# Kernel optimization log

Hardware: AMD Instinct MI355X
Metric: run time of the kernel (lower is better)

The kernel has to match this reference:

```python
import jax, jax.numpy as jnp
import numpy as np

H, N_EMB, D_EMB, D_UP = 1024, 8192, 512, 2048
B, T, BB, M, K_LABELS = 4, 4096, 512, 4096, 64


def _rms(x, w, eps=1e-6):
    xf = x.astype(jnp.float32)
    var = jnp.mean(xf * xf, axis=-1, keepdims=True)
    return (w * (xf * jax.lax.rsqrt(var + eps))).astype(x.dtype)


def setup_inputs() -> dict:
    key = jax.random.key(0)
    ks = jax.random.split(key, 8)
    bt = B * T
    inp = jax.random.normal(ks[0], (B, T, H), jnp.float32)
    w_k = jax.random.normal(ks[1], (N_EMB, H), jnp.float32) * 0.02
    w_v = jax.random.normal(ks[2], (N_EMB, D_EMB), jnp.float32) * 0.02
    w_up = jax.random.normal(ks[3], (D_UP, D_EMB), jnp.float32) * 0.02
    w_mix = jax.random.normal(ks[4], (H, D_UP + H), jnp.float32) * 0.02
    fw = jax.random.permutation(ks[5], bt)
    bw = jnp.argsort(fw)  # inverse permutation
    seq_sort = jax.random.randint(ks[6], (bt,), 0, K_LABELS)
    keep_cols = jnp.arange(M)  # keep first M of N_EMB rows
    emb_alloc = jnp.arange(N_EMB) % K_LABELS  # every label present among kept rows
    starts = jnp.zeros((bt,), jnp.int32)
    ends = jnp.full((bt,), M, jnp.int32)
    return {
        'input': inp, 'fw': fw, 'bw': bw, 'seq_sort': seq_sort,
        'keep_cols': keep_cols, 'emb_alloc': emb_alloc,
        'starts': starts, 'ends': ends, 'bb': BB,
        'w_k_weight': w_k, 'w_v_weight': w_v, 'w_up_weight': w_up,
        'w_mix_weight': w_mix,
        'norm_in_weight': jnp.ones((H,), jnp.float32),
        'norm_out_weight': jnp.ones((D_UP,), jnp.float32),
    }


def reference(input, fw, bw, seq_sort, keep_cols, emb_alloc, starts, ends, bb,
              w_k_weight, w_v_weight, w_up_weight, w_mix_weight,
              norm_in_weight, norm_out_weight):
    b, t, h = input.shape
    A = _rms(input, norm_in_weight)                      # [b,t,h]
    Bm = w_k_weight[keep_cols]                           # [m,h]
    Cm = w_v_weight[keep_cols]                           # [m,d_emb]
    la = emb_alloc[keep_cols]                            # [m]
    A = A.reshape(-1, h)[fw].reshape(-1, bb, h)          # [nb,bb,h]
    ss = seq_sort.reshape(-1, bb)                        # [nb,bb]
    st = starts.reshape(-1, bb).min(axis=-1)             # [nb]
    en = ends.reshape(-1, bb).max(axis=-1)               # [nb]
    # ragged per-block slice B[start:end] expressed as a kv range mask,
    # combined with the equality mask seq_sort[q] == emb_alloc[kv]
    scores = jnp.einsum('nqh,kh->nqk', A, Bm)            # [nb,bb,m]
    kv = jnp.arange(Bm.shape[0])
    mask = ((ss[:, :, None] == la[None, None, :])
            & (kv[None, None, :] >= st[:, None, None])
            & (kv[None, None, :] < en[:, None, None]))
    scores = jnp.where(mask, scores, -jnp.inf)
    p = jax.nn.softmax(scores, axis=-1)
    comb = jnp.einsum('nqk,kd->nqd', p, Cm)              # [nb,bb,d_emb]
    d_emb = Cm.shape[-1]
    comb = comb.reshape(-1, d_emb)[bw].reshape(b, t, d_emb)
    up = comb @ w_up_weight.T                            # [b,t,d_up]
    cat = jnp.concatenate([_rms(up, norm_out_weight), input], axis=-1)
    return cat @ w_mix_weight.T                          # [b,t,h]
```

## Files before the change

kernel.cpp:

```cpp
#include <hip/hip_runtime.h>
#include <hip/hip_bf16.h>
#include <cstdint>
#include <cstddef>

#define Hh 1024
#define D_EMB 512
#define D_UP 2048
#define BT 16384
#define BB_ 512
#define Mm 4096
#define NB 32
#define KL 64
#define NXCD 8
#define PMMAX 8192
#define QROWMAX 17408
#define MAXT 1088

typedef __attribute__((ext_vector_type(4))) float f4;
typedef __attribute__((ext_vector_type(4))) __bf16 bf4;
typedef __attribute__((ext_vector_type(8))) __bf16 bf8;
typedef __attribute__((ext_vector_type(4))) float f32x4;

__device__ __forceinline__ void gl_lds16(const void* g, void* l) {
  __builtin_amdgcn_global_load_lds((__attribute__((address_space(1))) void*)g,
                                   (__attribute__((address_space(3))) void*)l, 16, 0, 0);
}

__global__ __launch_bounds__(256) void conv_bf16_kernel(const float* __restrict__ src,
                                                        __bf16* __restrict__ dst, int n4) {
  int i = blockIdx.x * 256 + threadIdx.x;
  if (i >= n4) return;
  f4 v = ((const f4*)src)[i];
  bf4 o = {(__bf16)v[0], (__bf16)v[1], (__bf16)v[2], (__bf16)v[3]};
  ((bf4*)dst)[i] = o;
}

__global__ __launch_bounds__(256) void la_kernel(const int* __restrict__ keep,
                                                 const int* __restrict__ emb,
                                                 int* __restrict__ la, int m) {
  int i = blockIdx.x * 256 + threadIdx.x;
  if (i < m) la[i] = emb[keep[i]];
}

__global__ __launch_bounds__(256) void range_kernel(const int* __restrict__ starts,
                                                    const int* __restrict__ ends,
                                                    int* __restrict__ stA, int* __restrict__ enA) {
  int n = blockIdx.x;
  int t = threadIdx.x, lane = t & 63, wv = t >> 6;
  int s1 = min(starts[n * BB_ + t], starts[n * BB_ + t + 256]);
  int e1 = max(ends[n * BB_ + t], ends[n * BB_ + t + 256]);
#pragma unroll
  for (int off = 32; off; off >>= 1) {
    s1 = min(s1, __shfl_xor(s1, off));
    e1 = max(e1, __shfl_xor(e1, off));
  }
  __shared__ int ssh[4], esh[4];
  if (lane == 0) { ssh[wv] = s1; esh[wv] = e1; }
  __syncthreads();
  if (t == 0) {
    int s = ssh[0], e = esh[0];
#pragma unroll
    for (int k = 1; k < 4; ++k) { s = min(s, ssh[k]); e = max(e, esh[k]); }
    stA[n] = s; enA[n] = e;
  }
}

__global__ __launch_bounds__(256) void hist_kernel(const int* __restrict__ la,
                                                   int* __restrict__ goff) {
  __shared__ int cnt[KL];
  int tid = threadIdx.x;
  if (tid < KL) cnt[tid] = 0;
  __syncthreads();
  for (int k = tid; k < Mm; k += 256) atomicAdd(&cnt[la[k]], 1);
  __syncthreads();
  if (tid == 0) {
    int a = 0;
    for (int s = 0; s < KL; ++s) { goff[s] = a; a += cnt[s]; }
    goff[KL] = a;
  }
}

__global__ __launch_bounds__(256) void place_kernel(const int* __restrict__ la,
                                                    const int* __restrict__ keep,
                                                    const int* __restrict__ goff,
                                                    int* __restrict__ gk,
                                                    int* __restrict__ ridx) {
  int s = blockIdx.x;
  int tid = threadIdx.x, lane = tid & 63, wv = tid >> 6;
  __shared__ int wc[4];
  __shared__ int run;
  if (tid == 0) run = goff[s];
  __syncthreads();
  for (int base = 0; base < Mm; base += 256) {
    int k = base + tid;
    bool f = (la[k] == s);
    unsigned long long msk = __ballot(f);
    int myidx = __popcll(msk & ((1ull << lane) - 1ull));
    if (lane == 0) wc[wv] = __popcll(msk);
    __syncthreads();
    int woff = 0, tot = 0;
#pragma unroll
    for (int w = 0; w < 4; ++w) {
      if (w < wv) woff += wc[w];
      tot += wc[w];
    }
    int rbase = run;
    if (f) {
      int p = rbase + woff + myidx;
      gk[p] = k;
      ridx[p] = keep[k];
    }
    __syncthreads();
    if (tid == 0) run = rbase + tot;
    __syncthreads();
  }
}

__global__ __launch_bounds__(256) void qsort_kernel(const int* __restrict__ seq_sort,
                                                    int* __restrict__ qidx,
                                                    int* __restrict__ qoffA,
                                                    int* __restrict__ qcntA) {
  int n = blockIdx.x, tid = threadIdx.x;
  __shared__ int cnt[KL], pos[KL], pref[KL];
  if (tid < KL) cnt[tid] = 0;
  __syncthreads();
  int s0 = seq_sort[n * BB_ + tid];
  int s1 = seq_sort[n * BB_ + tid + 256];
  atomicAdd(&cnt[s0], 1);
  atomicAdd(&cnt[s1], 1);
  __syncthreads();
  if (tid == 0) {
    int a = 0;
    for (int s = 0; s < KL; ++s) { pref[s] = a; a += cnt[s]; }
  }
  __syncthreads();
  if (tid < KL) {
    pos[tid] = pref[tid];
    qoffA[n * KL + tid] = pref[tid];
    qcntA[n * KL + tid] = cnt[tid];
  }
  __syncthreads();
  int p0 = atomicAdd(&pos[s0], 1);
  qidx[n * BB_ + p0] = n * BB_ + tid;
  int p1 = atomicAdd(&pos[s1], 1);
  qidx[n * BB_ + p1] = n * BB_ + tid + 256;
}

__global__ __launch_bounds__(256) void qmeta_kernel(const int* __restrict__ qcntA,
                                                    const int* __restrict__ goff,
                                                    int* __restrict__ boff,
                                                    int* __restrict__ qtot,
                                                    int* __restrict__ ptq,
                                                    int* __restrict__ pb,
                                                    int* __restrict__ taskS,
                                                    int* __restrict__ taskT,
                                                    int* __restrict__ ntt,
                                                    int* __restrict__ pbTot) {
  int tid = threadIdx.x;
  if (tid < KL) {
    int s = tid, tot = 0;
    for (int n = 0; n < NB; ++n) { boff[n * KL + s] = tot; tot += qcntA[n * KL + s]; }
    qtot[s] = tot;
  }
  __syncthreads();
  if (tid == 0) {
    int tb = 0, tk = 0, pk = 0;
    for (int s = 0; s < KL; ++s) {
      ptq[s] = tb;
      int nt = (qtot[s] + 15) >> 4;
      for (int t2 = 0; t2 < nt; ++t2) { taskS[tk] = s; taskT[tk] = t2; ++tk; }
      tb += nt;
      pb[s] = pk;
      int cnt = goff[s + 1] - goff[s];
      pk += (cnt + 63) & ~63;
    }
    ptq[KL] = tb;
    ntt[0] = tk;
    pbTot[0] = pk;
  }
}

__global__ __launch_bounds__(256) void pridx_kernel(const int* __restrict__ goff,
                                                    const int* __restrict__ pb,
                                                    const int* __restrict__ ridx,
                                                    int* __restrict__ pridx) {
  int s = blockIdx.x;
  int cnt = goff[s + 1] - goff[s];
  int padded = (cnt + 63) & ~63;
  int base = pb[s];
  for (int i = threadIdx.x; i < padded; i += 256)
    pridx[base + i] = (i < cnt) ? ridx[goff[s] + i] : -1;
}

__global__ __launch_bounds__(256) void lohi_kernel(const int* __restrict__ gk,
                                                   const int* __restrict__ goff,
                                                   const int* __restrict__ pb,
                                                   const int* __restrict__ stA,
                                                   const int* __restrict__ enA,
                                                   int* __restrict__ loA, int* __restrict__ hiA) {
  int i = blockIdx.x * 256 + threadIdx.x;
  if (i >= NB * KL) return;
  int n = i / KL, s = i % KL;
  int b = goff[s], e = goff[s + 1];
  int st = stA[n], en = enA[n];
  int lo = b, hi = e;
  while (lo < hi) { int mid = (lo + hi) >> 1; if (gk[mid] < st) lo = mid + 1; else hi = mid; }
  int L = lo;
  lo = b; hi = e;
  while (lo < hi) { int mid = (lo + hi) >> 1; if (gk[mid] < en) lo = mid + 1; else hi = mid; }
  loA[i] = pb[s] + (L - goff[s]);
  hiA[i] = pb[s] + (lo - goff[s]);
}

__global__ __launch_bounds__(256) void gq_kernel(const int* __restrict__ qidx,
                                                 const int* __restrict__ qoffA,
                                                 const int* __restrict__ seq_sort,
                                                 const int* __restrict__ boff,
                                                 const int* __restrict__ ptq,
                                                 int* __restrict__ qg2, int* __restrict__ gq) {
  int e = blockIdx.x * 256 + threadIdx.x;
  int n = e >> 9;
  int q = qidx[e];
  int s = seq_sort[q];
  int i = (e & 511) - qoffA[n * KL + s];
  int gpos = ptq[s] * 16 + boff[n * KL + s] + i;
  qg2[gpos] = q;
  gq[q] = gpos;
}

__global__ __launch_bounds__(256) void qzero_kernel(const int* __restrict__ ptq,
                                                    const int* __restrict__ qtot,
                                                    __bf16* __restrict__ Qsw) {
  int s = blockIdx.x;
  int b0 = ptq[s] * 16 + qtot[s];
  int b1 = ptq[s + 1] * 16;
  bf8 z;
#pragma unroll
  for (int j = 0; j < 8; ++j) z[j] = (__bf16)0.f;
  for (int r = b0; r < b1; ++r)
    for (int e8 = threadIdx.x; e8 < 128; e8 += 256)
      *(bf8*)&Qsw[(size_t)r * 1024 + e8 * 8] = z;
}

__global__ __launch_bounds__(256) void kswb_kernel(const float* __restrict__ wk,
                                                   const int* __restrict__ pridx,
                                                   const int* __restrict__ pbTot,
                                                   __bf16* __restrict__ Ksw) {
  int pt = blockIdx.x;
  if (pt * 16 >= pbTot[0]) return;
  __shared__ __bf16 Tk[16][1040];
  int tid = threadIdx.x;
  int rr = tid >> 4, lt = tid & 15;
  int src = pridx[pt * 16 + rr];
  for (int cc = 0; cc < 16; ++cc) {
    int i4 = cc * 16 + lt;
    f4 v = {0.f, 0.f, 0.f, 0.f};
    if (src >= 0) v = ((const f4*)(wk + (size_t)src * Hh))[i4];
    bf4 o = {(__bf16)v[0], (__bf16)v[1], (__bf16)v[2], (__bf16)v[3]};
    *(bf4*)&Tk[rr][i4 * 4] = o;
  }
  __syncthreads();
#pragma unroll
  for (int i = 0; i < 8; ++i) {
    int f = tid + 256 * i;
    int ks = f >> 6, ln = f & 63;
    int c2 = ln & 15, rg2 = ln >> 4;
    bf8 o = *(const bf8*)&Tk[c2][ks * 32 + rg2 * 8];
    *(bf8*)&Ksw[(size_t)pt * 16384 + (size_t)f * 8] = o;
  }
}

__global__ __launch_bounds__(256) void vswb_kernel(const float* __restrict__ wv_,
                                                   const int* __restrict__ pridx,
                                                   const int* __restrict__ pbTot,
                                                   __bf16* __restrict__ Vsw) {
  int pblk = blockIdx.x;
  if (pblk * 32 >= pbTot[0]) return;
  __shared__ __bf16 Tv[32][528];
  int tid = threadIdx.x;
  int rr = tid >> 3, lt = tid & 7;
  int src = pridx[pblk * 32 + rr];
  for (int cc = 0; cc < 16; ++cc) {
    int i4 = cc * 8 + lt;
    f4 v = {0.f, 0.f, 0.f, 0.f};
    if (src >= 0) v = ((const f4*)(wv_ + (size_t)src * D_EMB))[i4];
    bf4 o = {(__bf16)v[0], (__bf16)v[1], (__bf16)v[2], (__bf16)v[3]};
    *(bf4*)&Tv[rr][i4 * 4] = o;
  }
  __syncthreads();
#pragma unroll
  for (int i = 0; i < 8; ++i) {
    int f = tid + 256 * i;
    int ff = f >> 6, ln = f & 63;
    int c2 = ln & 15, rg2 = ln >> 4;
    bf8 o;
#pragma unroll
    for (int j = 0; j < 8; ++j) o[j] = Tv[rg2 * 8 + j][ff * 16 + c2];
    *(bf8*)&Vsw[(size_t)pblk * 16384 + (size_t)f * 8] = o;
  }
}

__global__ __launch_bounds__(256) void rms_in_kernel(const float* __restrict__ input,
                                                     const int* __restrict__ bw,
                                                     const int* __restrict__ gq,
                                                     const float* __restrict__ wn,
                                                     __bf16* __restrict__ Qsw,
                                                     __bf16* __restrict__ inb) {
  __shared__ __align__(16) __bf16 rowbuf[4][1024];
  int wv = threadIdx.x >> 6, lane = threadIdx.x & 63;
  int j = blockIdx.x * 4 + wv;
  const f4* src = (const f4*)(input + (size_t)j * Hh);
  f4 v[4];
  float ss = 0.f;
#pragma unroll
  for (int c = 0; c < 4; ++c) {
    v[c] = src[c * 64 + lane];
    ss += v[c][0] * v[c][0] + v[c][1] * v[c][1] + v[c][2] * v[c][2] + v[c][3] * v[c][3];
  }
#pragma unroll
  for (int off = 32; off; off >>= 1) ss += __shfl_xor(ss, off);
  float sc = rsqrtf(ss * (1.f / Hh) + 1e-6f);
  bf4* dstI = (bf4*)(inb + (size_t)j * Hh);
#pragma unroll
  for (int c = 0; c < 4; ++c) {
    bf4 o = {(__bf16)v[c][0], (__bf16)v[c][1], (__bf16)v[c][2], (__bf16)v[c][3]};
    dstI[c * 64 + lane] = o;
  }
  const f4* w4 = (const f4*)wn;
#pragma unroll
  for (int c = 0; c < 4; ++c) {
    f4 w = w4[c * 64 + lane];
    bf4 o = {(__bf16)(v[c][0] * sc * w[0]), (__bf16)(v[c][1] * sc * w[1]),
             (__bf16)(v[c][2] * sc * w[2]), (__bf16)(v[c][3] * sc * w[3])};
    *(bf4*)&rowbuf[wv][(c * 64 + lane) * 4] = o;
  }
  int gpos = gq[bw[j]];
  int qt2 = gpos >> 4, cq = gpos & 15;
#pragma unroll
  for (int h = 0; h < 2; ++h) {
    int k_ = lane + h * 64;
    int ks = k_ >> 2, rg2 = k_ & 3;
    bf8 o = *(const bf8*)&rowbuf[wv][ks * 32 + rg2 * 8];
    *(bf8*)(Qsw + (size_t)qt2 * 16384 + ks * 512 + (cq + 16 * rg2) * 8) = o;
  }
}

__global__ __launch_bounds__(256, 3) void attn7_kernel(const __bf16* __restrict__ Qsw,
                                                       const __bf16* __restrict__ Ksw,
                                                       const __bf16* __restrict__ Vsw,
                                                       const int* __restrict__ qg2,
                                                       const int* __restrict__ qtot,
                                                       const int* __restrict__ ptq,
                                                       const int* __restrict__ taskS,
                                                       const int* __restrict__ taskT,
                                                       const int* __restrict__ nttA,
                                                       const int* __restrict__ pb,
                                                       const int* __restrict__ loP,
                                                       const int* __restrict__ hiP,
                                                       const int* __restrict__ fw,
                                                       __bf16* __restrict__ comb) {
  __shared__ float Sb[16][66];
  __shared__ __align__(16) __bf16 Plds[16][72];
  __shared__ float scl_s[16], lrec[16];
  __shared__ __align__(16) __bf16 owb[16][528];
  int t = blockIdx.x;
  if (t >= nttA[0]) return;
  int tid = threadIdx.x, wv = tid >> 6, lane = tid & 63;
  int c = lane & 15, rg = lane >> 4;
  int s = taskS[t], tl = taskT[t];
  int qtp = ptq[s] + tl;
  int qcnt = min(16, qtot[s] - tl * 16);
  bool qv = c < qcnt;
  int q_l = qg2[qtp * 16 + (qv ? c : 0)];
  int n_l = q_l >> 9;
  int lo_l = qv ? loP[n_l * KL + s] : 0x7fffffff;
  int hi_l = qv ? hiP[n_l * KL + s] : 0;
  int tlo = lo_l, thi = hi_l;
#pragma unroll
  for (int off = 1; off < 64; off <<= 1) {
    tlo = min(tlo, __shfl_xor(tlo, off));
    thi = max(thi, __shfl_xor(thi, off));
  }
  if (tlo >= thi) return;
  int pbs = pb[s];
  const __bf16* Qb = Qsw + (size_t)qtp * 16384 + lane * 8;

  float m[4] = {-1e30f, -1e30f, -1e30f, -1e30f};
  float l[4] = {0.f, 0.f, 0.f, 0.f};
  f32x4 acc[8];
  f32x4 zero = {0.f, 0.f, 0.f, 0.f};
#pragma unroll
  for (int tt = 0; tt < 8; ++tt) acc[tt] = zero;

  int p0beg = pbs + ((tlo - pbs) & ~63);
  for (int p0 = p0beg; p0 < thi; p0 += 64) {
    const __bf16* Kb = Ksw + (size_t)((p0 >> 4) + wv) * 16384 + lane * 8;
    f32x4 sacc = zero;
#pragma unroll
    for (int ks = 0; ks < 32; ++ks) {
      bf8 qf = *(const bf8*)(Qb + ks * 512);
      bf8 kf = *(const bf8*)(Kb + ks * 512);
      sacc = __builtin_amdgcn_mfma_f32_16x16x32_bf16(kf, qf, sacc, 0, 0, 0);
    }
#pragma unroll
    for (int r = 0; r < 4; ++r) {
      int kv = p0 + wv * 16 + rg * 4 + r;
      Sb[c][wv * 16 + rg * 4 + r] = (kv >= lo_l && kv < hi_l) ? sacc[r] : -1e30f;
    }
    __syncthreads();

#pragma unroll
    for (int r = 0; r < 4; ++r) {
      int q = wv * 4 + r;
      float sv = Sb[q][lane];
      float cm = sv;
#pragma unroll
      for (int off = 32; off; off >>= 1) cm = fmaxf(cm, __shfl_xor(cm, off));
      float mn = fmaxf(m[r], cm);
      float sc2 = __expf(m[r] - mn);
      float pv = __expf(sv - mn);
      float ssum = pv;
#pragma unroll
      for (int off = 32; off; off >>= 1) ssum += __shfl_xor(ssum, off);
      l[r] = l[r] * sc2 + ssum;
      m[r] = mn;
      Plds[q][lane] = (__bf16)pv;
      if (lane == 0) scl_s[q] = sc2;
    }
    __syncthreads();

    float sf = scl_s[c];
#pragma unroll
    for (int tt = 0; tt < 8; ++tt) acc[tt] = acc[tt] * sf;
    bf8 pa0 = *(const bf8*)&Plds[c][rg * 8];
    bf8 pa1 = *(const bf8*)&Plds[c][32 + rg * 8];
    const __bf16* Vb = Vsw + (size_t)(p0 >> 5) * 16384 + lane * 8;
#pragma unroll
    for (int tt = 0; tt < 8; ++tt) {
      int ff = wv * 8 + tt;
      bf8 v0 = *(const bf8*)(Vb + ff * 512);
      bf8 v1 = *(const bf8*)(Vb + 16384 + ff * 512);
      acc[tt] = __builtin_amdgcn_mfma_f32_16x16x32_bf16(v0, pa0, acc[tt], 0, 0, 0);
      acc[tt] = __builtin_amdgcn_mfma_f32_16x16x32_bf16(v1, pa1, acc[tt], 0, 0, 0);
    }
    __syncthreads();
  }

  if (lane == 0) {
#pragma unroll
    for (int r = 0; r < 4; ++r) lrec[wv * 4 + r] = l[r];
  }
  __syncthreads();
  float inv = 1.f / lrec[c];
#pragma unroll
  for (int tt = 0; tt < 8; ++tt) {
    bf4 o;
#pragma unroll
    for (int r = 0; r < 4; ++r) o[r] = (__bf16)(acc[tt][r] * inv);
    *(bf4*)&owb[c][(wv * 8 + tt) * 16 + rg * 4] = o;
  }
  __syncthreads();
#pragma unroll
  for (int r4 = 0; r4 < 4; ++r4) {
    int q2 = wv * 4 + r4;
    if (q2 < qcnt) {
      size_t ob = (size_t)fw[qg2[qtp * 16 + q2]] * D_EMB;
      *(bf8*)(comb + ob + lane * 8) = *(const bf8*)&owb[q2][lane * 8];
    }
  }
}

template <bool OUT_BF16>
__global__ __launch_bounds__(512, 2) void gemm9(const __bf16* __restrict__ x0, int k0,
                                                const __bf16* __restrict__ x1, int k1,
                                                const __bf16* __restrict__ w,
                                                void* __restrict__ outp, int Mt, int Nt) {
  __shared__ __align__(16) __bf16 lds[4][2][256 * 32];
  const int nwg = Mt * Nt;
  const int bid = blockIdx.x;
  const int swz = (bid % NXCD) * (nwg / NXCD) + bid / NXCD;
  const int m0 = (swz / Nt) * 256, n0 = (swz % Nt) * 256;
  const int K = k0 + k1;
  const int NT = K >> 5;
  const int N = Nt * 256;
  const int tid = threadIdx.x, lane = tid & 63, wvi = tid >> 6;
  const int wr = wvi >> 2, wc = wvi & 3;
  const int srow = tid >> 2;
  const int spb = (tid & 3) * 16;
  const int c = lane & 15, rg = lane >> 4;
  const int fa_off = c * 64 + ((rg ^ ((c >> 1) & 3)) << 4);

  auto stage = [&](int t) {
    int kg = t * 32;
    const __bf16* xs;
    int ld, kk;
    if (kg < k0) { xs = x0; ld = k0; kk = kg; }
    else         { xs = x1; ld = k1; kk = kg - k0; }
    int b = t & 3;
#pragma unroll
    for (int j = 0; j < 2; ++j) {
      int r = j * 128 + srow;
      int lcol = (spb ^ (((r >> 1) & 3) << 4)) >> 1;
      gl_lds16(xs + (size_t)(m0 + r) * ld + kk + lcol,
               (void*)((char*)&lds[b][0][0] + r * 64 + spb));
      gl_lds16(w + (size_t)(n0 + r) * K + kg + lcol,
               (void*)((char*)&lds[b][1][0] + r * 64 + spb));
    }
  };

  f32x4 acc[8][4];
  f32x4 zero = {0.f, 0.f, 0.f, 0.f};
#pragma unroll
  for (int a = 0; a < 8; ++a)
#pragma unroll
    for (int bnx = 0; bnx < 4; ++bnx) acc[a][bnx] = zero;

  auto compute = [&](int t) {
    const char* Ab = (const char*)&lds[t & 3][0][0];
    const char* Bb = (const char*)&lds[t & 3][1][0];
    bf8 afr[8], bfr[4];
#pragma unroll
    for (int fi = 0; fi < 8; ++fi)
      afr[fi] = *(const bf8*)(Ab + (wr * 128 + fi * 16) * 64 + fa_off);
#pragma unroll
    for (int ni = 0; ni < 4; ++ni)
      bfr[ni] = *(const bf8*)(Bb + (wc * 64 + ni * 16) * 64 + fa_off);
    __builtin_amdgcn_s_setprio(1);
#pragma unroll
    for (int fi = 0; fi < 8; ++fi)
#pragma unroll
      for (int ni = 0; ni < 4; ++ni)
        acc[fi][ni] = __builtin_amdgcn_mfma_f32_16x16x32_bf16(afr[fi], bfr[ni], acc[fi][ni], 0, 0, 0);
    __builtin_amdgcn_s_setprio(0);
  };

  stage(0); stage(1); stage(2);
  asm volatile("s_waitcnt vmcnt(8)" ::: "memory");
  __builtin_amdgcn_s_barrier();

  for (int t = 0; t < NT - 3; ++t) {
    stage(t + 3);
    compute(t);
    asm volatile("s_waitcnt vmcnt(8)" ::: "memory");
    __builtin_amdgcn_s_barrier();
  }
  compute(NT - 3);
  asm volatile("s_waitcnt vmcnt(4)" ::: "memory");
  __builtin_amdgcn_s_barrier();
  compute(NT - 2);
  asm volatile("s_waitcnt vmcnt(0)" ::: "memory");
  __builtin_amdgcn_s_barrier();
  compute(NT - 1);

  const int r0 = (lane >> 4) * 4, cc = lane & 15;
#pragma unroll
  for (int mi = 0; mi < 8; ++mi) {
    int rowb = m0 + wr * 128 + mi * 16 + r0;
#pragma unroll
    for (int ni = 0; ni < 4; ++ni) {
      int col = n0 + wc * 64 + ni * 16 + cc;
#pragma unroll
      for (int r = 0; r < 4; ++r) {
        float v = acc[mi][ni][r];
        if (OUT_BF16)
          ((__bf16*)outp)[(size_t)(rowb + r) * N + col] = (__bf16)v;
        else
          ((float*)outp)[(size_t)(rowb + r) * N + col] = v;
      }
    }
  }
}

__global__ __launch_bounds__(256) void rms_up_kernel(__bf16* __restrict__ up,
                                                     const float* __restrict__ wn) {
  int wv = threadIdx.x >> 6, lane = threadIdx.x & 63;
  size_t j = (size_t)blockIdx.x * 4 + wv;
  bf8* row = (bf8*)(up + j * D_UP);
  bf8 v[4];
  float ss = 0.f;
#pragma unroll
  for (int c = 0; c < 4; ++c) {
    v[c] = row[c * 64 + lane];
#pragma unroll
    for (int i = 0; i < 8; ++i) { float f = (float)v[c][i]; ss += f * f; }
  }
#pragma unroll
  for (int off = 32; off; off >>= 1) ss += __shfl_xor(ss, off);
  float sc = rsqrtf(ss * (1.f / D_UP) + 1e-6f);
#pragma unroll
  for (int c = 0; c < 4; ++c) {
    int ebase = (c * 64 + lane) * 8;
    f4 wa = *(const f4*)(wn + ebase);
    f4 wb = *(const f4*)(wn + ebase + 4);
    bf8 o;
#pragma unroll
    for (int i = 0; i < 4; ++i) o[i] = (__bf16)((float)v[c][i] * sc * wa[i]);
#pragma unroll
    for (int i = 0; i < 4; ++i) o[4 + i] = (__bf16)((float)v[c][4 + i] * sc * wb[i]);
    row[c * 64 + lane] = o;
  }
}

extern "C" void kernel_launch(void* const* d_in, const int* in_sizes, int n_in, void* d_out,
                              int out_size, void* d_ws, size_t ws_size, hipStream_t stream) {
  const float* input = (const float*)d_in[0];
  const int* fw = (const int*)d_in[1];
  const int* bw = (const int*)d_in[2];
  const int* seq_sort = (const int*)d_in[3];
  const int* keep_cols = (const int*)d_in[4];
  const int* emb_alloc = (const int*)d_in[5];
  const int* starts = (const int*)d_in[6];
  const int* ends = (const int*)d_in[7];
  const float* w_k = (const float*)d_in[9];
  const float* w_v = (const float*)d_in[10];
  const float* w_up = (const float*)d_in[11];
  const float* w_mix = (const float*)d_in[12];
  const float* w_nin = (const float*)d_in[13];
  const float* w_nout = (const float*)d_in[14];

  char* p = (char*)d_ws;
  auto take = [&](size_t b) {
    void* r = (void*)p;
    p += (b + 255) & ~(size_t)255;
    return r;
  };
  __bf16* inb = (__bf16*)take((size_t)BT * Hh * 2);
  __bf16* comb = (__bf16*)take((size_t)BT * D_EMB * 2);
  __bf16* wupB = (__bf16*)take((size_t)D_UP * D_EMB * 2);
  __bf16* wmixB = (__bf16*)take((size_t)Hh * (D_UP + Hh) * 2);
  char* pB = p;
  __bf16* Ksw = (__bf16*)take((size_t)PMMAX * 1024 * 2);
  __bf16* Vsw = (__bf16*)take((size_t)PMMAX * 512 * 2);
  __bf16* Qsw = (__bf16*)take((size_t)QROWMAX * 1024 * 2);
  int* la = (int*)take(Mm * 4);
  int* stA = (int*)take(NB * 4);
  int* enA = (int*)take(NB * 4);
  int* goff = (int*)take((KL + 1) * 4);
  int* gk = (int*)take(Mm * 4);
  int* ridx = (int*)take(Mm * 4);
  int* pridx = (int*)take(PMMAX * 4);
  int* loA = (int*)take(NB * KL * 4);
  int* hiA = (int*)take(NB * KL * 4);
  int* qidx = (int*)take(BT * 4);
  int* qoffA = (int*)take(NB * KL * 4);
  int* qcntA = (int*)take(NB * KL * 4);
  int* boff = (int*)take(NB * KL * 4);
  int* qtot = (int*)take(KL * 4);
  int* ptq = (int*)take((KL + 1) * 4);
  int* pb = (int*)take(KL * 4);
  int* taskS = (int*)take(MAXT * 4);
  int* taskT = (int*)take(MAXT * 4);
  int* ntt = (int*)take(4);
  int* pbTot = (int*)take(4);
  int* qg2 = (int*)take(QROWMAX * 4);
  int* gq = (int*)take(BT * 4);
  __bf16* up = (__bf16*)pB;

  conv_bf16_kernel<<<(D_UP * D_EMB / 4 + 255) / 256, 256, 0, stream>>>(w_up, wupB, D_UP * D_EMB / 4);
  conv_bf16_kernel<<<(Hh * (D_UP + Hh) / 4 + 255) / 256, 256, 0, stream>>>(w_mix, wmixB,
                                                                           Hh * (D_UP + Hh) / 4);
  la_kernel<<<Mm / 256, 256, 0, stream>>>(keep_cols, emb_alloc, la, Mm);
  range_kernel<<<NB, 256, 0, stream>>>(starts, ends, stA, enA);
  hist_kernel<<<1, 256, 0, stream>>>(la, goff);
  qsort_kernel<<<NB, 256, 0, stream>>>(seq_sort, qidx, qoffA, qcntA);
  place_kernel<<<KL, 256, 0, stream>>>(la, keep_cols, goff, gk, ridx);
  qmeta_kernel<<<1, 256, 0, stream>>>(qcntA, goff, boff, qtot, ptq, pb, taskS, taskT, ntt, pbTot);
  pridx_kernel<<<KL, 256, 0, stream>>>(goff, pb, ridx, pridx);
  lohi_kernel<<<(NB * KL + 255) / 256, 256, 0, stream>>>(gk, goff, pb, stA, enA, loA, hiA);
  gq_kernel<<<BT / 256, 256, 0, stream>>>(qidx, qoffA, seq_sort, boff, ptq, qg2, gq);
  qzero_kernel<<<KL, 256, 0, stream>>>(ptq, qtot, Qsw);
  kswb_kernel<<<PMMAX / 16, 256, 0, stream>>>(w_k, pridx, pbTot, Ksw);
  vswb_kernel<<<PMMAX / 32, 256, 0, stream>>>(w_v, pridx, pbTot, Vsw);

  rms_in_kernel<<<BT / 4, 256, 0, stream>>>(input, bw, gq, w_nin, Qsw, inb);
  attn7_kernel<<<MAXT, 256, 0, stream>>>(Qsw, Ksw, Vsw, qg2, qtot, ptq, taskS, taskT, ntt, pb,
                                         loA, hiA, fw, comb);
  gemm9<true><<<BT / 256 * (D_UP / 256), 512, 0, stream>>>(comb, D_EMB, (const __bf16*)nullptr, 0,
                                                           wupB, (void*)up, BT / 256, D_UP / 256);
  rms_up_kernel<<<BT / 4, 256, 0, stream>>>(up, w_nout);
  gemm9<false><<<BT / 256 * (Hh / 256), 512, 0, stream>>>(up, D_UP, inb, Hh, wmixB, d_out,
                                                          BT / 256, Hh / 256);
}
```

Baseline: 384.8 us.

## Fuse RMS of up-projection into GEMM epilogue/prologue and merge small setup kernels

The separate rms_up pass is removed. The up GEMM now accumulates per-row sums of squares with atomics in its epilogue, the norm_out weight is folded into the bf16 copy of w_mix, and the mix GEMM scales its accumulators by the row rsqrt after the tile covering the up segment. Many tiny setup kernels are merged into a few multi-role launches to cut launch overhead. The risk is a precision difference, because the sums of squares come from fp32 accumulators before bf16 rounding, plus atomic contention on the row sums.

After: 342.4 us. 1.12x faster.

```diff
diff --git a/kernel.cpp b/kernel.cpp
--- a/kernel.cpp
+++ b/kernel.cpp
@@ -26,57 +26,125 @@
                                    (__attribute__((address_space(3))) void*)l, 16, 0, 0);
 }
 
-__global__ __launch_bounds__(256) void conv_bf16_kernel(const float* __restrict__ src,
-                                                        __bf16* __restrict__ dst, int n4) {
-  int i = blockIdx.x * 256 + threadIdx.x;
-  if (i >= n4) return;
-  f4 v = ((const f4*)src)[i];
-  bf4 o = {(__bf16)v[0], (__bf16)v[1], (__bf16)v[2], (__bf16)v[3]};
-  ((bf4*)dst)[i] = o;
-}
-
-__global__ __launch_bounds__(256) void la_kernel(const int* __restrict__ keep,
-                                                 const int* __restrict__ emb,
-                                                 int* __restrict__ la, int m) {
-  int i = blockIdx.x * 256 + threadIdx.x;
-  if (i < m) la[i] = emb[keep[i]];
-}
-
-__global__ __launch_bounds__(256) void range_kernel(const int* __restrict__ starts,
-                                                    const int* __restrict__ ends,
-                                                    int* __restrict__ stA, int* __restrict__ enA) {
-  int n = blockIdx.x;
-  int t = threadIdx.x, lane = t & 63, wv = t >> 6;
-  int s1 = min(starts[n * BB_ + t], starts[n * BB_ + t + 256]);
-  int e1 = max(ends[n * BB_ + t], ends[n * BB_ + t + 256]);
-#pragma unroll
-  for (int off = 32; off; off >>= 1) {
-    s1 = min(s1, __shfl_xor(s1, off));
-    e1 = max(e1, __shfl_xor(e1, off));
-  }
+__global__ __launch_bounds__(256) void k1_misc(const float* __restrict__ w_up,
+                                               const float* __restrict__ w_mix,
+                                               const float* __restrict__ w_nout,
+                                               const int* __restrict__ keep,
+                                               const int* __restrict__ emb,
+                                               const int* __restrict__ starts,
+                                               const int* __restrict__ ends,
+                                               const int* __restrict__ seq_sort,
+                                               __bf16* __restrict__ wupB,
+                                               __bf16* __restrict__ wmixB,
+                                               int* __restrict__ la,
+                                               int* __restrict__ stA, int* __restrict__ enA,
+                                               int* __restrict__ qidx,
+                                               int* __restrict__ qoffA, int* __restrict__ qcntA,
+                                               float* __restrict__ rowssq) {
   __shared__ int ssh[4], esh[4];
-  if (lane == 0) { ssh[wv] = s1; esh[wv] = e1; }
-  __syncthreads();
-  if (t == 0) {
-    int s = ssh[0], e = esh[0];
-#pragma unroll
-    for (int k = 1; k < 4; ++k) { s = min(s, ssh[k]); e = max(e, esh[k]); }
-    stA[n] = s; enA[n] = e;
-  }
-}
-
-__global__ __launch_bounds__(256) void hist_kernel(const int* __restrict__ la,
-                                                   int* __restrict__ goff) {
+  __shared__ int cnt[KL], pos[KL], pref[KL];
+  int b = blockIdx.x, tid = threadIdx.x;
+  if (b < 1024) {
+    int i = b * 256 + tid;
+    f4 v = ((const f4*)w_up)[i];
+    bf4 o = {(__bf16)v[0], (__bf16)v[1], (__bf16)v[2], (__bf16)v[3]};
+    ((bf4*)wupB)[i] = o;
+  } else if (b < 4096) {
+    int i = (b - 1024) * 256 + tid;
+    f4 v = ((const f4*)w_mix)[i];
+    int kq = i % 768;
+    if (kq < 512) {
+      f4 wn = ((const f4*)w_nout)[kq];
+      v[0] *= wn[0]; v[1] *= wn[1]; v[2] *= wn[2]; v[3] *= wn[3];
+    }
+    bf4 o = {(__bf16)v[0], (__bf16)v[1], (__bf16)v[2], (__bf16)v[3]};
+    ((bf4*)wmixB)[i] = o;
+  } else if (b < 4112) {
+    int i = (b - 4096) * 256 + tid;
+    if (i < Mm) la[i] = emb[keep[i]];
+  } else if (b < 4144) {
+    int n = b - 4112;
+    int lane = tid & 63, wv = tid >> 6;
+    int s1 = min(starts[n * BB_ + tid], starts[n * BB_ + tid + 256]);
+    int e1 = max(ends[n * BB_ + tid], ends[n * BB_ + tid + 256]);
+#pragma unroll
+    for (int off = 32; off; off >>= 1) {
+      s1 = min(s1, __shfl_xor(s1, off));
+      e1 = max(e1, __shfl_xor(e1, off));
+    }
+    if (lane == 0) { ssh[wv] = s1; esh[wv] = e1; }
+    __syncthreads();
+    if (tid == 0) {
+      int s = ssh[0], e = esh[0];
+#pragma unroll
+      for (int k = 1; k < 4; ++k) { s = min(s, ssh[k]); e = max(e, esh[k]); }
+      stA[n] = s; enA[n] = e;
+    }
+  } else if (b < 4176) {
+    int n = b - 4144;
+    if (tid < KL) cnt[tid] = 0;
+    __syncthreads();
+    int s0 = seq_sort[n * BB_ + tid];
+    int s1 = seq_sort[n * BB_ + tid + 256];
+    atomicAdd(&cnt[s0], 1);
+    atomicAdd(&cnt[s1], 1);
+    __syncthreads();
+    if (tid == 0) {
+      int a = 0;
+      for (int s = 0; s < KL; ++s) { pref[s] = a; a += cnt[s]; }
+    }
+    __syncthreads();
+    if (tid < KL) {
+      pos[tid] = pref[tid];
+      qoffA[n * KL + tid] = pref[tid];
+      qcntA[n * KL + tid] = cnt[tid];
+    }
+    __syncthreads();
+    int p0 = atomicAdd(&pos[s0], 1);
+    qidx[n * BB_ + p0] = n * BB_ + tid;
+    int p1 = atomicAdd(&pos[s1], 1);
+    qidx[n * BB_ + p1] = n * BB_ + tid + 256;
+  } else {
+    int i = (b - 4176) * 256 + tid;
+    if (i < 4096) { f4 z = {0.f, 0.f, 0.f, 0.f}; ((f4*)rowssq)[i] = z; }
+  }
+}
+
+__global__ __launch_bounds__(256) void k2_meta(const int* __restrict__ la,
+                                               const int* __restrict__ qcntA,
+                                               int* __restrict__ goff,
+                                               int* __restrict__ boff, int* __restrict__ qtot,
+                                               int* __restrict__ ptq, int* __restrict__ pb,
+                                               int* __restrict__ taskS, int* __restrict__ taskT,
+                                               int* __restrict__ ntt, int* __restrict__ pbTot) {
   __shared__ int cnt[KL];
   int tid = threadIdx.x;
   if (tid < KL) cnt[tid] = 0;
   __syncthreads();
   for (int k = tid; k < Mm; k += 256) atomicAdd(&cnt[la[k]], 1);
+  if (tid < KL) {
+    int s = tid, tot = 0;
+    for (int n = 0; n < NB; ++n) { boff[n * KL + s] = tot; tot += qcntA[n * KL + s]; }
+    qtot[s] = tot;
+  }
   __syncthreads();
   if (tid == 0) {
     int a = 0;
     for (int s = 0; s < KL; ++s) { goff[s] = a; a += cnt[s]; }
     goff[KL] = a;
+    int tb = 0, tk = 0, pk = 0;
+    for (int s = 0; s < KL; ++s) {
+      ptq[s] = tb;
+      int nt = (qtot[s] + 15) >> 4;
+      for (int t2 = 0; t2 < nt; ++t2) { taskS[tk] = s; taskT[tk] = t2; ++tk; }
+      tb += nt;
+      pb[s] = pk;
+      int c2 = goff[s + 1] - goff[s];
+      pk += (c2 + 63) & ~63;
+    }
+    ptq[KL] = tb;
+    ntt[0] = tk;
+    pbTot[0] = pk;
   }
 }
 
@@ -116,187 +184,120 @@
   }
 }
 
-__global__ __launch_bounds__(256) void qsort_kernel(const int* __restrict__ seq_sort,
-                                                    int* __restrict__ qidx,
-                                                    int* __restrict__ qoffA,
-                                                    int* __restrict__ qcntA) {
-  int n = blockIdx.x, tid = threadIdx.x;
-  __shared__ int cnt[KL], pos[KL], pref[KL];
-  if (tid < KL) cnt[tid] = 0;
-  __syncthreads();
-  int s0 = seq_sort[n * BB_ + tid];
-  int s1 = seq_sort[n * BB_ + tid + 256];
-  atomicAdd(&cnt[s0], 1);
-  atomicAdd(&cnt[s1], 1);
-  __syncthreads();
-  if (tid == 0) {
-    int a = 0;
-    for (int s = 0; s < KL; ++s) { pref[s] = a; a += cnt[s]; }
-  }
-  __syncthreads();
-  if (tid < KL) {
-    pos[tid] = pref[tid];
-    qoffA[n * KL + tid] = pref[tid];
-    qcntA[n * KL + tid] = cnt[tid];
-  }
-  __syncthreads();
-  int p0 = atomicAdd(&pos[s0], 1);
-  qidx[n * BB_ + p0] = n * BB_ + tid;
-  int p1 = atomicAdd(&pos[s1], 1);
-  qidx[n * BB_ + p1] = n * BB_ + tid + 256;
-}
-
-__global__ __launch_bounds__(256) void qmeta_kernel(const int* __restrict__ qcntA,
-                                                    const int* __restrict__ goff,
-                                                    int* __restrict__ boff,
-                                                    int* __restrict__ qtot,
-                                                    int* __restrict__ ptq,
-                                                    int* __restrict__ pb,
-                                                    int* __restrict__ taskS,
-                                                    int* __restrict__ taskT,
-                                                    int* __restrict__ ntt,
-                                                    int* __restrict__ pbTot) {
-  int tid = threadIdx.x;
-  if (tid < KL) {
-    int s = tid, tot = 0;
-    for (int n = 0; n < NB; ++n) { boff[n * KL + s] = tot; tot += qcntA[n * KL + s]; }
-    qtot[s] = tot;
-  }
-  __syncthreads();
-  if (tid == 0) {
-    int tb = 0, tk = 0, pk = 0;
-    for (int s = 0; s < KL; ++s) {
-      ptq[s] = tb;
-      int nt = (qtot[s] + 15) >> 4;
-      for (int t2 = 0; t2 < nt; ++t2) { taskS[tk] = s; taskT[tk] = t2; ++tk; }
-      tb += nt;
-      pb[s] = pk;
-      int cnt = goff[s + 1] - goff[s];
-      pk += (cnt + 63) & ~63;
-    }
-    ptq[KL] = tb;
-    ntt[0] = tk;
-    pbTot[0] = pk;
-  }
-}
-
-__global__ __launch_bounds__(256) void pridx_kernel(const int* __restrict__ goff,
-                                                    const int* __restrict__ pb,
-                                                    const int* __restrict__ ridx,
-                                                    int* __restrict__ pridx) {
-  int s = blockIdx.x;
-  int cnt = goff[s + 1] - goff[s];
-  int padded = (cnt + 63) & ~63;
-  int base = pb[s];
-  for (int i = threadIdx.x; i < padded; i += 256)
-    pridx[base + i] = (i < cnt) ? ridx[goff[s] + i] : -1;
-}
-
-__global__ __launch_bounds__(256) void lohi_kernel(const int* __restrict__ gk,
-                                                   const int* __restrict__ goff,
-                                                   const int* __restrict__ pb,
-                                                   const int* __restrict__ stA,
-                                                   const int* __restrict__ enA,
-                                                   int* __restrict__ loA, int* __restrict__ hiA) {
-  int i = blockIdx.x * 256 + threadIdx.x;
-  if (i >= NB * KL) return;
-  int n = i / KL, s = i % KL;
-  int b = goff[s], e = goff[s + 1];
-  int st = stA[n], en = enA[n];
-  int lo = b, hi = e;
-  while (lo < hi) { int mid = (lo + hi) >> 1; if (gk[mid] < st) lo = mid + 1; else hi = mid; }
-  int L = lo;
-  lo = b; hi = e;
-  while (lo < hi) { int mid = (lo + hi) >> 1; if (gk[mid] < en) lo = mid + 1; else hi = mid; }
-  loA[i] = pb[s] + (L - goff[s]);
-  hiA[i] = pb[s] + (lo - goff[s]);
-}
-
-__global__ __launch_bounds__(256) void gq_kernel(const int* __restrict__ qidx,
-                                                 const int* __restrict__ qoffA,
-                                                 const int* __restrict__ seq_sort,
-                                                 const int* __restrict__ boff,
-                                                 const int* __restrict__ ptq,
-                                                 int* __restrict__ qg2, int* __restrict__ gq) {
-  int e = blockIdx.x * 256 + threadIdx.x;
-  int n = e >> 9;
-  int q = qidx[e];
-  int s = seq_sort[q];
-  int i = (e & 511) - qoffA[n * KL + s];
-  int gpos = ptq[s] * 16 + boff[n * KL + s] + i;
-  qg2[gpos] = q;
-  gq[q] = gpos;
-}
-
-__global__ __launch_bounds__(256) void qzero_kernel(const int* __restrict__ ptq,
-                                                    const int* __restrict__ qtot,
-                                                    __bf16* __restrict__ Qsw) {
-  int s = blockIdx.x;
-  int b0 = ptq[s] * 16 + qtot[s];
-  int b1 = ptq[s + 1] * 16;
-  bf8 z;
-#pragma unroll
-  for (int j = 0; j < 8; ++j) z[j] = (__bf16)0.f;
-  for (int r = b0; r < b1; ++r)
-    for (int e8 = threadIdx.x; e8 < 128; e8 += 256)
-      *(bf8*)&Qsw[(size_t)r * 1024 + e8 * 8] = z;
-}
-
-__global__ __launch_bounds__(256) void kswb_kernel(const float* __restrict__ wk,
-                                                   const int* __restrict__ pridx,
-                                                   const int* __restrict__ pbTot,
-                                                   __bf16* __restrict__ Ksw) {
-  int pt = blockIdx.x;
-  if (pt * 16 >= pbTot[0]) return;
-  __shared__ __bf16 Tk[16][1040];
-  int tid = threadIdx.x;
-  int rr = tid >> 4, lt = tid & 15;
-  int src = pridx[pt * 16 + rr];
-  for (int cc = 0; cc < 16; ++cc) {
-    int i4 = cc * 16 + lt;
-    f4 v = {0.f, 0.f, 0.f, 0.f};
-    if (src >= 0) v = ((const f4*)(wk + (size_t)src * Hh))[i4];
-    bf4 o = {(__bf16)v[0], (__bf16)v[1], (__bf16)v[2], (__bf16)v[3]};
-    *(bf4*)&Tk[rr][i4 * 4] = o;
-  }
-  __syncthreads();
-#pragma unroll
-  for (int i = 0; i < 8; ++i) {
-    int f = tid + 256 * i;
-    int ks = f >> 6, ln = f & 63;
-    int c2 = ln & 15, rg2 = ln >> 4;
-    bf8 o = *(const bf8*)&Tk[c2][ks * 32 + rg2 * 8];
-    *(bf8*)&Ksw[(size_t)pt * 16384 + (size_t)f * 8] = o;
-  }
-}
-
-__global__ __launch_bounds__(256) void vswb_kernel(const float* __restrict__ wv_,
-                                                   const int* __restrict__ pridx,
-                                                   const int* __restrict__ pbTot,
-                                                   __bf16* __restrict__ Vsw) {
-  int pblk = blockIdx.x;
-  if (pblk * 32 >= pbTot[0]) return;
-  __shared__ __bf16 Tv[32][528];
-  int tid = threadIdx.x;
-  int rr = tid >> 3, lt = tid & 7;
-  int src = pridx[pblk * 32 + rr];
-  for (int cc = 0; cc < 16; ++cc) {
-    int i4 = cc * 8 + lt;
-    f4 v = {0.f, 0.f, 0.f, 0.f};
-    if (src >= 0) v = ((const f4*)(wv_ + (size_t)src * D_EMB))[i4];
-    bf4 o = {(__bf16)v[0], (__bf16)v[1], (__bf16)v[2], (__bf16)v[3]};
-    *(bf4*)&Tv[rr][i4 * 4] = o;
-  }
-  __syncthreads();
-#pragma unroll
-  for (int i = 0; i < 8; ++i) {
-    int f = tid + 256 * i;
-    int ff = f >> 6, ln = f & 63;
-    int c2 = ln & 15, rg2 = ln >> 4;
-    bf8 o;
-#pragma unroll
-    for (int j = 0; j < 8; ++j) o[j] = Tv[rg2 * 8 + j][ff * 16 + c2];
-    *(bf8*)&Vsw[(size_t)pblk * 16384 + (size_t)f * 8] = o;
+__global__ __launch_bounds__(256) void k4_idx(const int* __restrict__ goff,
+                                              const int* __restrict__ pb,
+                                              const int* __restrict__ ridx,
+                                              int* __restrict__ pridx,
+                                              const int* __restrict__ gk,
+                                              const int* __restrict__ stA,
+                                              const int* __restrict__ enA,
+                                              int* __restrict__ loA, int* __restrict__ hiA,
+                                              const int* __restrict__ qidx,
+                                              const int* __restrict__ qoffA,
+                                              const int* __restrict__ seq_sort,
+                                              const int* __restrict__ boff,
+                                              const int* __restrict__ ptq,
+                                              int* __restrict__ qg2, int* __restrict__ gq,
+                                              const int* __restrict__ qtot,
+                                              __bf16* __restrict__ Qsw) {
+  int b = blockIdx.x, tid = threadIdx.x;
+  if (b < 64) {
+    int s = b;
+    int cnt2 = goff[s + 1] - goff[s];
+    int padded = (cnt2 + 63) & ~63;
+    int base = pb[s];
+    for (int i = tid; i < padded; i += 256)
+      pridx[base + i] = (i < cnt2) ? ridx[goff[s] + i] : -1;
+  } else if (b < 72) {
+    int i = (b - 64) * 256 + tid;
+    if (i < NB * KL) {
+      int n = i / KL, s = i % KL;
+      int b0 = goff[s], e0 = goff[s + 1];
+      int st = stA[n], en = enA[n];
+      int lo = b0, hi = e0;
+      while (lo < hi) { int mid = (lo + hi) >> 1; if (gk[mid] < st) lo = mid + 1; else hi = mid; }
+      int L = lo;
+      lo = b0; hi = e0;
+      while (lo < hi) { int mid = (lo + hi) >> 1; if (gk[mid] < en) lo = mid + 1; else hi = mid; }
+      loA[i] = pb[s] + (L - goff[s]);
+      hiA[i] = pb[s] + (lo - goff[s]);
+    }
+  } else if (b < 136) {
+    int e = (b - 72) * 256 + tid;
+    int n = e >> 9;
+    int q = qidx[e];
+    int s = seq_sort[q];
+    int i = (e & 511) - qoffA[n * KL + s];
+    int gpos = ptq[s] * 16 + boff[n * KL + s] + i;
+    qg2[gpos] = q;
+    gq[q] = gpos;
+  } else {
+    int s = b - 136;
+    int b0 = ptq[s] * 16 + qtot[s];
+    int b1 = ptq[s + 1] * 16;
+    bf8 z;
+#pragma unroll
+    for (int j = 0; j < 8; ++j) z[j] = (__bf16)0.f;
+    for (int r = b0; r < b1; ++r)
+      for (int e8 = tid; e8 < 128; e8 += 256)
+        *(bf8*)&Qsw[(size_t)r * 1024 + e8 * 8] = z;
+  }
+}
+
+__global__ __launch_bounds__(256) void k5_build(const float* __restrict__ wk,
+                                                const float* __restrict__ wv_,
+                                                const int* __restrict__ pridx,
+                                                const int* __restrict__ pbTot,
+                                                __bf16* __restrict__ Ksw,
+                                                __bf16* __restrict__ Vsw) {
+  __shared__ __align__(16) char shb[33792];
+  int b = blockIdx.x, tid = threadIdx.x;
+  if (b < 512) {
+    int pt = b;
+    if (pt * 16 >= pbTot[0]) return;
+    auto Tk = (__bf16(*)[1040])shb;
+    int rr = tid >> 4, lt = tid & 15;
+    int src = pridx[pt * 16 + rr];
+    for (int cc = 0; cc < 16; ++cc) {
+      int i4 = cc * 16 + lt;
+      f4 v = {0.f, 0.f, 0.f, 0.f};
+      if (src >= 0) v = ((const f4*)(wk + (size_t)src * Hh))[i4];
+      bf4 o = {(__bf16)v[0], (__bf16)v[1], (__bf16)v[2], (__bf16)v[3]};
+      *(bf4*)&Tk[rr][i4 * 4] = o;
+    }
+    __syncthreads();
+#pragma unroll
+    for (int i = 0; i < 8; ++i) {
+      int f = tid + 256 * i;
+      int ks = f >> 6, ln = f & 63;
+      int c2 = ln & 15, rg2 = ln >> 4;
+      bf8 o = *(const bf8*)&Tk[c2][ks * 32 + rg2 * 8];
+      *(bf8*)&Ksw[(size_t)pt * 16384 + (size_t)f * 8] = o;
+    }
+  } else {
+    int pblk = b - 512;
+    if (pblk * 32 >= pbTot[0]) return;
+    auto Tv = (__bf16(*)[528])shb;
+    int rr = tid >> 3, lt = tid & 7;
+    int src = pridx[pblk * 32 + rr];
+    for (int cc = 0; cc < 16; ++cc) {
+      int i4 = cc * 8 + lt;
+      f4 v = {0.f, 0.f, 0.f, 0.f};
+      if (src >= 0) v = ((const f4*)(wv_ + (size_t)src * D_EMB))[i4];
+      bf4 o = {(__bf16)v[0], (__bf16)v[1], (__bf16)v[2], (__bf16)v[3]};
+      *(bf4*)&Tv[rr][i4 * 4] = o;
+    }
+    __syncthreads();
+#pragma unroll
+    for (int i = 0; i < 8; ++i) {
+      int f = tid + 256 * i;
+      int ff = f >> 6, ln = f & 63;
+      int c2 = ln & 15, rg2 = ln >> 4;
+      bf8 o;
+#pragma unroll
+      for (int j = 0; j < 8; ++j) o[j] = Tv[rg2 * 8 + j][ff * 16 + c2];
+      *(bf8*)&Vsw[(size_t)pblk * 16384 + (size_t)f * 8] = o;
+    }
   }
 }
 
@@ -470,11 +471,12 @@
   }
 }
 
-template <bool OUT_BF16>
-__global__ __launch_bounds__(512, 2) void gemm9(const __bf16* __restrict__ x0, int k0,
-                                                const __bf16* __restrict__ x1, int k1,
-                                                const __bf16* __restrict__ w,
-                                                void* __restrict__ outp, int Mt, int Nt) {
+template <bool OUT_BF16, bool SSQ, bool RS>
+__global__ __launch_bounds__(512, 2) void gemm10(const __bf16* __restrict__ x0, int k0,
+                                                 const __bf16* __restrict__ x1, int k1,
+                                                 const __bf16* __restrict__ w,
+                                                 void* __restrict__ outp, int Mt, int Nt,
+                                                 float* __restrict__ rowssq, int rsTile) {
   __shared__ __align__(16) __bf16 lds[4][2][256 * 32];
   const int nwg = Mt * Nt;
   const int bid = blockIdx.x;
@@ -489,6 +491,7 @@
   const int spb = (tid & 3) * 16;
   const int c = lane & 15, rg = lane >> 4;
   const int fa_off = c * 64 + ((rg ^ ((c >> 1) & 3)) << 4);
+  const int r0 = (lane >> 4) * 4;
 
   auto stage = [&](int t) {
     int kg = t * 32;
@@ -534,6 +537,19 @@
     __builtin_amdgcn_s_setprio(0);
   };
 
+  auto apply_rs = [&]() {
+#pragma unroll
+    for (int mi = 0; mi < 8; ++mi) {
+      int base = m0 + wr * 128 + mi * 16 + r0;
+#pragma unroll
+      for (int r = 0; r < 4; ++r) {
+        float rsv = rsqrtf(rowssq[base + r] * (1.f / 2048.f) + 1e-6f);
+#pragma unroll
+        for (int ni = 0; ni < 4; ++ni) acc[mi][ni][r] *= rsv;
+      }
+    }
+  };
+
   stage(0); stage(1); stage(2);
   asm volatile("s_waitcnt vmcnt(8)" ::: "memory");
   __builtin_amdgcn_s_barrier();
@@ -541,18 +557,44 @@
   for (int t = 0; t < NT - 3; ++t) {
     stage(t + 3);
     compute(t);
+    if (RS) { if (t == rsTile) apply_rs(); }
     asm volatile("s_waitcnt vmcnt(8)" ::: "memory");
     __builtin_amdgcn_s_barrier();
   }
   compute(NT - 3);
+  if (RS) { if (NT - 3 == rsTile) apply_rs(); }
   asm volatile("s_waitcnt vmcnt(4)" ::: "memory");
   __builtin_amdgcn_s_barrier();
   compute(NT - 2);
+  if (RS) { if (NT - 2 == rsTile) apply_rs(); }
   asm volatile("s_waitcnt vmcnt(0)" ::: "memory");
   __builtin_amdgcn_s_barrier();
   compute(NT - 1);
 
-  const int r0 = (lane >> 4) * 4, cc = lane & 15;
+  if (SSQ) {
+#pragma unroll
+    for (int mi = 0; mi < 8; ++mi) {
+      float p[4];
+#pragma unroll
+      for (int r = 0; r < 4; ++r) {
+        float a = 0.f;
+#pragma unroll
+        for (int ni = 0; ni < 4; ++ni) a += acc[mi][ni][r] * acc[mi][ni][r];
+        p[r] = a;
+      }
+#pragma unroll
+      for (int off = 1; off < 16; off <<= 1)
+#pragma unroll
+        for (int r = 0; r < 4; ++r) p[r] += __shfl_xor(p[r], off);
+      if ((lane & 15) == 0) {
+        int base = m0 + wr * 128 + mi * 16 + r0;
+#pragma unroll
+        for (int r = 0; r < 4; ++r) atomicAdd(&rowssq[base + r], p[r]);
+      }
+    }
+  }
+
+  const int cc = lane & 15;
 #pragma unroll
   for (int mi = 0; mi < 8; ++mi) {
     int rowb = m0 + wr * 128 + mi * 16 + r0;
@@ -568,36 +610,6 @@
           ((float*)outp)[(size_t)(rowb + r) * N + col] = v;
       }
     }
-  }
-}
-
-__global__ __launch_bounds__(256) void rms_up_kernel(__bf16* __restrict__ up,
-                                                     const float* __restrict__ wn) {
-  int wv = threadIdx.x >> 6, lane = threadIdx.x & 63;
-  size_t j = (size_t)blockIdx.x * 4 + wv;
-  bf8* row = (bf8*)(up + j * D_UP);
-  bf8 v[4];
-  float ss = 0.f;
-#pragma unroll
-  for (int c = 0; c < 4; ++c) {
-    v[c] = row[c * 64 + lane];
-#pragma unroll
-    for (int i = 0; i < 8; ++i) { float f = (float)v[c][i]; ss += f * f; }
-  }
-#pragma unroll
-  for (int off = 32; off; off >>= 1) ss += __shfl_xor(ss, off);
-  float sc = rsqrtf(ss * (1.f / D_UP) + 1e-6f);
-#pragma unroll
-  for (int c = 0; c < 4; ++c) {
-    int ebase = (c * 64 + lane) * 8;
-    f4 wa = *(const f4*)(wn + ebase);
-    f4 wb = *(const f4*)(wn + ebase + 4);
-    bf8 o;
-#pragma unroll
-    for (int i = 0; i < 4; ++i) o[i] = (__bf16)((float)v[c][i] * sc * wa[i]);
-#pragma unroll
-    for (int i = 0; i < 4; ++i) o[4 + i] = (__bf16)((float)v[c][4 + i] * sc * wb[i]);
-    row[c * 64 + lane] = o;
   }
 }
 
@@ -628,6 +640,7 @@
   __bf16* comb = (__bf16*)take((size_t)BT * D_EMB * 2);
   __bf16* wupB = (__bf16*)take((size_t)D_UP * D_EMB * 2);
   __bf16* wmixB = (__bf16*)take((size_t)Hh * (D_UP + Hh) * 2);
+  float* rowssq = (float*)take((size_t)BT * 4);
   char* pB = p;
   __bf16* Ksw = (__bf16*)take((size_t)PMMAX * 1024 * 2);
   __bf16* Vsw = (__bf16*)take((size_t)PMMAX * 512 * 2);
@@ -656,28 +669,19 @@
   int* gq = (int*)take(BT * 4);
   __bf16* up = (__bf16*)pB;
 
-  conv_bf16_kernel<<<(D_UP * D_EMB / 4 + 255) / 256, 256, 0, stream>>>(w_up, wupB, D_UP * D_EMB / 4);
-  conv_bf16_kernel<<<(Hh * (D_UP + Hh) / 4 + 255) / 256, 256, 0, stream>>>(w_mix, wmixB,
-                                                                           Hh * (D_UP + Hh) / 4);
-  la_kernel<<<Mm / 256, 256, 0, stream>>>(keep_cols, emb_alloc, la, Mm);
-  range_kernel<<<NB, 256, 0, stream>>>(starts, ends, stA, enA);
-  hist_kernel<<<1, 256, 0, stream>>>(la, goff);
-  qsort_kernel<<<NB, 256, 0, stream>>>(seq_sort, qidx, qoffA, qcntA);
+  k1_misc<<<4192, 256, 0, stream>>>(w_up, w_mix, w_nout, keep_cols, emb_alloc, starts, ends,
+                                    seq_sort, wupB, wmixB, la, stA, enA, qidx, qoffA, qcntA,
+                                    rowssq);
+  k2_meta<<<1, 256, 0, stream>>>(la, qcntA, goff, boff, qtot, ptq, pb, taskS, taskT, ntt, pbTot);
   place_kernel<<<KL, 256, 0, stream>>>(la, keep_cols, goff, gk, ridx);
-  qmeta_kernel<<<1, 256, 0, stream>>>(qcntA, goff, boff, qtot, ptq, pb, taskS, taskT, ntt, pbTot);
-  pridx_kernel<<<KL, 256, 0, stream>>>(goff, pb, ridx, pridx);
-  lohi_kernel<<<(NB * KL + 255) / 256, 256, 0, stream>>>(gk, goff, pb, stA, enA, loA, hiA);
-  gq_kernel<<<BT / 256, 256, 0, stream>>>(qidx, qoffA, seq_sort, boff, ptq, qg2, gq);
-  qzero_kernel<<<KL, 256, 0, stream>>>(ptq, qtot, Qsw);
-  kswb_kernel<<<PMMAX / 16, 256, 0, stream>>>(w_k, pridx, pbTot, Ksw);
-  vswb_kernel<<<PMMAX / 32, 256, 0, stream>>>(w_v, pridx, pbTot, Vsw);
-
+  k4_idx<<<200, 256, 0, stream>>>(goff, pb, ridx, pridx, gk, stA, enA, loA, hiA, qidx, qoffA,
+                                  seq_sort, boff, ptq, qg2, gq, qtot, Qsw);
+  k5_build<<<768, 256, 0, stream>>>(w_k, w_v, pridx, pbTot, Ksw, Vsw);
   rms_in_kernel<<<BT / 4, 256, 0, stream>>>(input, bw, gq, w_nin, Qsw, inb);
   attn7_kernel<<<MAXT, 256, 0, stream>>>(Qsw, Ksw, Vsw, qg2, qtot, ptq, taskS, taskT, ntt, pb,
                                          loA, hiA, fw, comb);
-  gemm9<true><<<BT / 256 * (D_UP / 256), 512, 0, stream>>>(comb, D_EMB, (const __bf16*)nullptr, 0,
-                                                           wupB, (void*)up, BT / 256, D_UP / 256);
-  rms_up_kernel<<<BT / 4, 256, 0, stream>>>(up, w_nout);
-  gemm9<false><<<BT / 256 * (Hh / 256), 512, 0, stream>>>(up, D_UP, inb, Hh, wmixB, d_out,
-                                                          BT / 256, Hh / 256);
-}
+  gemm10<true, true, false><<<BT / 256 * (D_UP / 256), 512, 0, stream>>>(
+      comb, D_EMB, (const __bf16*)nullptr, 0, wupB, (void*)up, BT / 256, D_UP / 256, rowssq, -1);
+  gemm10<false, false, true><<<BT / 256 * (Hh / 256), 512, 0, stream>>>(
+      up, D_UP, inb, Hh, wmixB, d_out, BT / 256, Hh / 256, rowssq, 63);
+}
```
